# Kernel optimization log

Hardware: AMD Instinct MI355X
Metric: run time of the kernel (lower is better)

Reference implementation:

```python
import jax, jax.numpy as jnp
import numpy as np

N_NODES, FEAT_DIM, EMBED_DIM, BATCH, N_NEIGH = 200000, 128, 64, 8192, 64


def setup_inputs() -> dict:
    key = jax.random.key(0)
    k0, k1, k2, k3, k4, k5 = jax.random.split(key, 6)
    return {
        "features_table": jax.random.normal(k0, (N_NODES, FEAT_DIM), jnp.float32),
        # xavier-uniform-like scale for [2*feat_dim, embed_dim]
        "weight": jax.random.normal(k1, (2 * FEAT_DIM, EMBED_DIM), jnp.float32)
        * (1.0 / np.sqrt(2 * FEAT_DIM)),
        "nodes": jax.random.randint(k2, (BATCH,), 0, N_NODES),
        "batch_scores": jax.random.normal(k3, (BATCH, 2), jnp.float32),
        "neigh_scores": jax.random.normal(k4, (BATCH, N_NEIGH, 2), jnp.float32),
        "neighs_ids": jax.random.randint(k5, (BATCH, N_NEIGH), 0, N_NODES),
        "num_sample": 16,
    }


def reference(features_table, weight, nodes, batch_scores, neigh_scores, neighs_ids, num_sample):
    # |center_score - neigh_score| per candidate neighbor  -> [B, K]
    score_diff = jnp.abs(batch_scores[:, :1] - neigh_scores[:, :, 0])
    # keep num_sample neighbors with SMALLEST score diff (top_k on negated diffs)
    neg_top, sel_idx = jax.lax.top_k(-score_diff, num_sample)  # [B, k]
    samp_scores = -neg_top  # selected (ascending-ish) score diffs, as in choose_step_test
    sel_ids = jnp.take_along_axis(neighs_ids, sel_idx, axis=1)  # [B, k]
    # masked-mean aggregation == mean of the k selected neighbor features
    neigh_feats = features_table[sel_ids]            # [B, k, F]
    agg_feats = neigh_feats.mean(axis=1)             # [B, F]
    self_feats = features_table[nodes]               # [B, F]
    cat_feats = jnp.concatenate([self_feats, agg_feats], axis=1)  # [B, 2F]
    to_feats = jax.nn.relu(cat_feats @ weight)       # [B, E]
    return to_feats, samp_scores
```

## Files before the change

kernel.cpp:

```cpp
#include <hip/hip_runtime.h>

#define BATCH   8192
#define NNEIGH  64
#define FEAT    128
#define EMBED   64
#define ROWS    8
#define CATP    260
#define EPAD    68
#define KCHUNKS 8

__global__ __launch_bounds__(256, 4) void intra_agg_kernel(
    const float* __restrict__ feat,
    const float* __restrict__ W,
    const int*   __restrict__ nodes,
    const float* __restrict__ bscore,
    const float* __restrict__ nscore,
    const int*   __restrict__ nids,
    const int*   __restrict__ ns_ptr,
    float*       __restrict__ out)
{
    const int b0   = blockIdx.x * ROWS;
    const int tid  = threadIdx.x;
    const int lane = tid & 63;
    const int wave = tid >> 6;
    const int ns   = *ns_ptr;

    __shared__ int   s_sel[ROWS][NNEIGH];
    __shared__ float s_cat[ROWS * CATP];
    __shared__ float s_part[KCHUNKS][ROWS][EPAD];

    {
        float d[2];
        int   idx[2];
        #pragma unroll
        for (int i = 0; i < 2; ++i) {
            const int row = b0 + wave * 2 + i;
            const float  ctr = bscore[row * 2];
            const float2 sc  = *(const float2*)&nscore[(size_t)(row * NNEIGH + lane) * 2];
            d[i]   = fabsf(ctr - sc.x);
            idx[i] = lane;
        }
        #pragma unroll
        for (int i = 0; i < 2; ++i) {
            #pragma unroll
            for (int k = 2; k <= 64; k <<= 1) {
                #pragma unroll
                for (int j = k >> 1; j > 0; j >>= 1) {
                    const float od = __shfl_xor(d[i], j);
                    const int   oi = __shfl_xor(idx[i], j);
                    const bool up    = ((lane & k) == 0);
                    const bool lower = ((lane & j) == 0);
                    const bool oless = (od < d[i]) || (od == d[i] && oi < idx[i]);
                    if ((lower == up) ? oless : !oless) { d[i] = od; idx[i] = oi; }
                }
            }
        }
        #pragma unroll
        for (int i = 0; i < 2; ++i) {
            const int r   = wave * 2 + i;
            const int row = b0 + r;
            if (lane < ns) {
                out[(size_t)BATCH * EMBED + (size_t)row * ns + lane] = d[i];
                s_sel[r][lane] = nids[row * NNEIGH + idx[i]];
            }
        }
    }
    __syncthreads();

    {
        const int r   = tid >> 5;
        const int c   = tid & 31;
        const int row = b0 + r;
        const float inv_ns = 1.0f / (float)ns;
        float4 a = make_float4(0.f, 0.f, 0.f, 0.f);
        if (ns == 16) {
            #pragma unroll
            for (int j = 0; j < 16; ++j) {
                const float4 v = *(const float4*)&feat[(size_t)s_sel[r][j] * FEAT + c * 4];
                a.x += v.x; a.y += v.y; a.z += v.z; a.w += v.w;
            }
        } else {
            for (int j = 0; j < ns; ++j) {
                const float4 v = *(const float4*)&feat[(size_t)s_sel[r][j] * FEAT + c * 4];
                a.x += v.x; a.y += v.y; a.z += v.z; a.w += v.w;
            }
        }
        const float4 sf = *(const float4*)&feat[(size_t)nodes[row] * FEAT + c * 4];
        *(float4*)&s_cat[r * CATP + c * 4] = sf;
        a.x *= inv_ns; a.y *= inv_ns; a.z *= inv_ns; a.w *= inv_ns;
        *(float4*)&s_cat[r * CATP + FEAT + c * 4] = a;
    }
    __syncthreads();

    {
        const int q  = tid & 15;
        const int rq = (tid >> 4) & 1;
        const int ks = tid >> 5;
        const int k0 = ks * 32;

        float4 acc[4];
        #pragma unroll
        for (int r = 0; r < 4; ++r) acc[r] = make_float4(0.f, 0.f, 0.f, 0.f);

        #pragma unroll
        for (int kk = 0; kk < 32; kk += 4) {
            const int k = k0 + kk;
            float4 cv[4];
            #pragma unroll
            for (int r = 0; r < 4; ++r)
                cv[r] = *(const float4*)&s_cat[(rq * 4 + r) * CATP + k];
            #pragma unroll
            for (int t = 0; t < 4; ++t) {
                const float4 w4 = *(const float4*)&W[(size_t)(k + t) * EMBED + q * 4];
                #pragma unroll
                for (int r = 0; r < 4; ++r) {
                    const float cf = (t == 0) ? cv[r].x : (t == 1) ? cv[r].y
                                   : (t == 2) ? cv[r].z : cv[r].w;
                    acc[r].x += cf * w4.x; acc[r].y += cf * w4.y;
                    acc[r].z += cf * w4.z; acc[r].w += cf * w4.w;
                }
            }
        }
        #pragma unroll
        for (int r = 0; r < 4; ++r)
            *(float4*)&s_part[ks][rq * 4 + r][q * 4] = acc[r];
    }
    __syncthreads();

    if (tid < ROWS * 16) {
        const int r2 = tid >> 4;
        const int q  = tid & 15;
        float4 o = make_float4(0.f, 0.f, 0.f, 0.f);
        #pragma unroll
        for (int p = 0; p < KCHUNKS; ++p) {
            const float4 v = *(const float4*)&s_part[p][r2][q * 4];
            o.x += v.x; o.y += v.y; o.z += v.z; o.w += v.w;
        }
        o.x = fmaxf(o.x, 0.f); o.y = fmaxf(o.y, 0.f);
        o.z = fmaxf(o.z, 0.f); o.w = fmaxf(o.w, 0.f);
        *(float4*)&out[(size_t)(b0 + r2) * EMBED + q * 4] = o;
    }
}

extern "C" void kernel_launch(void* const* d_in, const int* in_sizes, int n_in,
                              void* d_out, int out_size, void* d_ws, size_t ws_size,
                              hipStream_t stream) {
    const float* feat   = (const float*)d_in[0];
    const float* W      = (const float*)d_in[1];
    const int*   nodes  = (const int*)d_in[2];
    const float* bscore = (const float*)d_in[3];
    const float* nscore = (const float*)d_in[4];
    const int*   nids   = (const int*)d_in[5];
    const int*   nsamp  = (const int*)d_in[6];
    float* out = (float*)d_out;

    intra_agg_kernel<<<BATCH / ROWS, 256, 0, stream>>>(feat, W, nodes, bscore,
                                                       nscore, nids, nsamp, out);
}
```

Measured before the change: 24.27 us.

## Keep top-k selection and gather within each wave, removing shared-memory handoff

Each wave now gathers features for the same two rows it sorted. Selected neighbor ids are broadcast with wave shuffles instead of being staged in shared memory, which removes one block-wide barrier and the s_sel buffer. The self-feature load is issued at kernel start so it overlaps the bitonic sort, and the two rows' sort networks are interleaved for more instruction-level parallelism. The cost is extra shuffles per gather step and higher register pressure.

```diff
diff --git a/kernel.cpp b/kernel.cpp
--- a/kernel.cpp
+++ b/kernel.cpp
@@ -7,7 +7,7 @@
 #define ROWS    8
 #define CATP    260
 #define EPAD    68
-#define KCHUNKS 8
+#define KCH     8
 
 __global__ __launch_bounds__(256, 4) void intra_agg_kernel(
     const float* __restrict__ feat,
@@ -25,69 +25,76 @@
     const int wave = tid >> 6;
     const int ns   = *ns_ptr;
 
-    __shared__ int   s_sel[ROWS][NNEIGH];
     __shared__ float s_cat[ROWS * CATP];
-    __shared__ float s_part[KCHUNKS][ROWS][EPAD];
+    __shared__ float s_part[KCH][ROWS][EPAD];
 
-    {
-        float d[2];
-        int   idx[2];
+    const int r0   = wave * 2;
+    const int half = lane >> 5;
+    const int c    = lane & 31;
+
+    const int    selfnode = nodes[b0 + r0 + half];
+    const float4 self4    = *(const float4*)&feat[(size_t)selfnode * FEAT + c * 4];
+
+    float d[2];
+    int   idx[2];
+    #pragma unroll
+    for (int i = 0; i < 2; ++i) {
+        const int row = b0 + r0 + i;
+        const float  ctr = bscore[row * 2];
+        const float2 sc  = *(const float2*)&nscore[(size_t)(row * NNEIGH + lane) * 2];
+        d[i]   = fabsf(ctr - sc.x);
+        idx[i] = lane;
+    }
+    #pragma unroll
+    for (int k = 2; k <= 64; k <<= 1) {
         #pragma unroll
-        for (int i = 0; i < 2; ++i) {
-            const int row = b0 + wave * 2 + i;
-            const float  ctr = bscore[row * 2];
-            const float2 sc  = *(const float2*)&nscore[(size_t)(row * NNEIGH + lane) * 2];
-            d[i]   = fabsf(ctr - sc.x);
-            idx[i] = lane;
-        }
-        #pragma unroll
-        for (int i = 0; i < 2; ++i) {
+        for (int j = k >> 1; j > 0; j >>= 1) {
             #pragma unroll
-            for (int k = 2; k <= 64; k <<= 1) {
-                #pragma unroll
-                for (int j = k >> 1; j > 0; j >>= 1) {
-                    const float od = __shfl_xor(d[i], j);
-                    const int   oi = __shfl_xor(idx[i], j);
-                    const bool up    = ((lane & k) == 0);
-                    const bool lower = ((lane & j) == 0);
-                    const bool oless = (od < d[i]) || (od == d[i] && oi < idx[i]);
-                    if ((lower == up) ? oless : !oless) { d[i] = od; idx[i] = oi; }
-                }
-            }
-        }
-        #pragma unroll
-        for (int i = 0; i < 2; ++i) {
-            const int r   = wave * 2 + i;
-            const int row = b0 + r;
-            if (lane < ns) {
-                out[(size_t)BATCH * EMBED + (size_t)row * ns + lane] = d[i];
-                s_sel[r][lane] = nids[row * NNEIGH + idx[i]];
+            for (int i = 0; i < 2; ++i) {
+                const float od = __shfl_xor(d[i], j);
+                const int   oi = __shfl_xor(idx[i], j);
+                const bool up    = ((lane & k) == 0);
+                const bool lower = ((lane & j) == 0);
+                const bool oless = (od < d[i]) || (od == d[i] && oi < idx[i]);
+                if ((lower == up) ? oless : !oless) { d[i] = od; idx[i] = oi; }
             }
         }
     }
-    __syncthreads();
+    int gid[2] = {0, 0};
+    #pragma unroll
+    for (int i = 0; i < 2; ++i) {
+        const int row = b0 + r0 + i;
+        if (lane < ns) {
+            out[(size_t)BATCH * EMBED + (size_t)row * ns + lane] = d[i];
+            gid[i] = nids[row * NNEIGH + idx[i]];
+        }
+    }
+
+    float4 a = make_float4(0.f, 0.f, 0.f, 0.f);
+    if (ns == 16) {
+        #pragma unroll
+        for (int j = 0; j < 16; ++j) {
+            const int id0 = __shfl(gid[0], j);
+            const int id1 = __shfl(gid[1], j);
+            const int id  = half ? id1 : id0;
+            const float4 v = *(const float4*)&feat[(size_t)id * FEAT + c * 4];
+            a.x += v.x; a.y += v.y; a.z += v.z; a.w += v.w;
+        }
+    } else {
+        for (int j = 0; j < ns; ++j) {
+            const int id0 = __shfl(gid[0], j);
+            const int id1 = __shfl(gid[1], j);
+            const int id  = half ? id1 : id0;
+            const float4 v = *(const float4*)&feat[(size_t)id * FEAT + c * 4];
+            a.x += v.x; a.y += v.y; a.z += v.z; a.w += v.w;
+        }
+    }
+    const float inv_ns = 1.0f / (float)ns;
+    a.x *= inv_ns; a.y *= inv_ns; a.z *= inv_ns; a.w *= inv_ns;
 
     {
-        const int r   = tid >> 5;
-        const int c   = tid & 31;
-        const int row = b0 + r;
-        const float inv_ns = 1.0f / (float)ns;
-        float4 a = make_float4(0.f, 0.f, 0.f, 0.f);
-        if (ns == 16) {
-            #pragma unroll
-            for (int j = 0; j < 16; ++j) {
-                const float4 v = *(const float4*)&feat[(size_t)s_sel[r][j] * FEAT + c * 4];
-                a.x += v.x; a.y += v.y; a.z += v.z; a.w += v.w;
-            }
-        } else {
-            for (int j = 0; j < ns; ++j) {
-                const float4 v = *(const float4*)&feat[(size_t)s_sel[r][j] * FEAT + c * 4];
-                a.x += v.x; a.y += v.y; a.z += v.z; a.w += v.w;
-            }
-        }
-        const float4 sf = *(const float4*)&feat[(size_t)nodes[row] * FEAT + c * 4];
-        *(float4*)&s_cat[r * CATP + c * 4] = sf;
-        a.x *= inv_ns; a.y *= inv_ns; a.z *= inv_ns; a.w *= inv_ns;
+        const int r = r0 + half;
+        *(float4*)&s_cat[r * CATP + c * 4]        = self4;
         *(float4*)&s_cat[r * CATP + FEAT + c * 4] = a;
     }
     __syncthreads();
@@ -132,7 +139,7 @@
         const int q  = tid & 15;
         float4 o = make_float4(0.f, 0.f, 0.f, 0.f);
         #pragma unroll
-        for (int p = 0; p < KCHUNKS; ++p) {
+        for (int p = 0; p < KCH; ++p) {
             const float4 v = *(const float4*)&s_part[p][r2][q * 4];
             o.x += v.x; o.y += v.y; o.z += v.z; o.w += v.w;
         }
```

Measured after the change: 23.91 us. No clear change (-1.5%).
